# Kernel tuning notes

Measured on AMD Instinct MI355X. Metric: run time of the kernel, lower is better.

The kernel has to match this reference:

```python
import jax, jax.numpy as jnp
import numpy as np
from jax import lax

B, L, D_MODEL = 2, 4096, 1024
D_INNER = 2 * D_MODEL          # expand=2
D_STATE = D_INNER              # required: complex einsum contracts d_inner vs d_state
DT_RANK = 64                   # ceil(1024/16)
D_CONV = 4


def setup_inputs() -> dict:
    key = jax.random.key(0)
    ks = jax.random.split(key, 16)
    s = lambda *sh: 1.0 / np.sqrt(sh[-1])
    return {
        "hidden_states": jax.random.normal(ks[0], (B, L, D_MODEL), jnp.float32),
        "delta": jax.random.normal(ks[1], (B, L, DT_RANK), jnp.float32),
        # in_proj: Linear(d_model -> 2*d_inner), no bias
        "in_proj_w": jax.random.normal(ks[2], (2 * D_INNER, D_MODEL), jnp.float32) * s(D_MODEL),
        # depthwise causal conv1d: (out=d_inner, in/groups=1, k)
        "conv_w": jax.random.normal(ks[3], (D_INNER, 1, D_CONV), jnp.float32) * s(D_CONV),
        "conv_b": jax.random.normal(ks[4], (D_INNER,), jnp.float32) * 0.01,
        # ComplexStateSpace: only A_real affects the real output (x is real)
        "A_real": jax.random.normal(ks[5], (D_STATE, D_STATE), jnp.float32) * 0.1 / np.sqrt(D_STATE),
        # MIMO linears (torch Linear weight layout [out, in])
        "B_w": jax.random.normal(ks[6], (D_STATE, D_INNER), jnp.float32) * 0.1 * s(D_INNER),
        "C_w": jax.random.normal(ks[7], (D_INNER, D_STATE), jnp.float32) * 0.1 * s(D_STATE),
        "D_w": jax.random.normal(ks[8], (D_INNER, D_INNER), jnp.float32) * 0.1 * s(D_INNER),
        # SelectiveScan params
        "dt_proj_w": jax.random.normal(ks[9], (D_INNER, DT_RANK), jnp.float32) * 0.01,
        "dt_proj_b": jax.random.normal(ks[10], (D_INNER,), jnp.float32) * 0.01,
        "A_log": jax.random.uniform(ks[11], (D_INNER,), jnp.float32, -4.0, -1.0),
        "D_ss": jnp.ones((D_INNER,), jnp.float32),
        # out_proj: Linear(d_inner -> d_model), no bias
        "out_proj_w": jax.random.normal(ks[12], (D_MODEL, D_INNER), jnp.float32) * s(D_INNER),
    }


def reference(hidden_states, delta, in_proj_w, conv_w, conv_b, A_real,
              B_w, C_w, D_w, dt_proj_w, dt_proj_b, A_log, D_ss, out_proj_w):
    d_inner = A_log.shape[0]
    # in_proj + split
    xz = jnp.einsum('bld,ed->ble', hidden_states, in_proj_w)
    x, z = xz[..., :d_inner], xz[..., d_inner:]
    # depthwise causal conv1d (left-pad k-1 == torch pad both + truncate to L)
    xc = jnp.swapaxes(x, 1, 2)                      # [b, d, l]
    xc = lax.conv_general_dilated(xc, conv_w, window_strides=(1,),
                                  padding=[(D_CONV - 1, 0)],
                                  feature_group_count=d_inner)
    x = jnp.swapaxes(xc, 1, 2) + conv_b             # [b, l, d]
    x = jax.nn.silu(x)
    # ComplexStateSpace: real part of (x @ (A_real + iA_imag)) == x @ A_real
    x = x + jnp.einsum('bls,st->blt', x, A_real)
    # MIMO SSM: state_t = cumsum(B x)_t ; y_t = C state_t + D x_t  (vectorized)
    Bx = jnp.einsum('bld,sd->bls', x, B_w)          # [b, l, d_state]
    states = jnp.cumsum(Bx, axis=1)
    x_mimo = jnp.einsum('bls,es->ble', states, C_w) + jnp.einsum('bld,ed->ble', x, D_w)
    x = x + x_mimo
    # SelectiveScan: state = state * exp(dlt * A) + u, A = -exp(A_log)
    dlt = jax.nn.softplus(jnp.einsum('blr,dr->bld', delta, dt_proj_w) + dt_proj_b)
    decay = jnp.exp(dlt * (-jnp.exp(A_log)))        # [b, l, d], in (0, 1)

    def step(state, inp):
        dec, u = inp
        state = state * dec + u
        return state, state

    init = jnp.zeros_like(x[:, 0])
    _, scan_states = lax.scan(step, init,
                              (jnp.swapaxes(decay, 0, 1), jnp.swapaxes(x, 0, 1)))
    x = jnp.swapaxes(scan_states, 0, 1) + x * D_ss
    # gate + out projection
    out = x * jax.nn.silu(z)
    return jnp.einsum('ble,de->bld', out, out_proj_w)
```

## Files before the change

### kernel.cpp

```cpp
#include <hip/hip_runtime.h>
#include <cstdint>
#include <cstddef>


typedef unsigned short u16;
typedef __bf16 bf16x8 __attribute__((ext_vector_type(8)));
typedef float  f32x4  __attribute__((ext_vector_type(4)));

#define BDIM 256
#define M_ROWS 8192
#define LSEQ   4096
#define DI     2048
#define NCH    64
#define CLEN   64

__device__ __forceinline__ float bf2f(u16 h) {
    return __uint_as_float(((unsigned int)h) << 16);
}
__device__ __forceinline__ u16 f2bf(float f) {
    unsigned int u = __float_as_uint(f);
    u = u + 0x7fffu + ((u >> 16) & 1u);
    return (u16)(u >> 16);
}
__device__ __forceinline__ float siluf(float v) { return v / (1.0f + expf(-v)); }

__device__ __forceinline__ void load16_to_lds(const u16* g, u16* l) {
    __builtin_amdgcn_global_load_lds((const __attribute__((address_space(1))) void*)g,
                                     (__attribute__((address_space(3))) void*)l,
                                     16, 0, 0);
}

__global__ void k_cvt_all(const float* __restrict__ hs, const float* __restrict__ inproj,
                          const float* __restrict__ Bw, const float* __restrict__ Cw,
                          const float* __restrict__ outw, const float* __restrict__ delta,
                          const float* __restrict__ dtw,
                          u16* __restrict__ XH, u16* __restrict__ W1, u16* __restrict__ WBb,
                          u16* __restrict__ WC, u16* __restrict__ WO, u16* __restrict__ DLT,
                          u16* __restrict__ WDT) {
    long i = (long)(blockIdx.x * BDIM + threadIdx.x) * 4;
    const float* src; u16* dst; long off;
    if      (i <  8388608L) { src = hs;     dst = XH;  off = 0L; }
    else if (i < 12582912L) { src = inproj; dst = W1;  off = 8388608L; }
    else if (i < 16777216L) { src = Bw;     dst = WBb; off = 12582912L; }
    else if (i < 20971520L) { src = Cw;     dst = WC;  off = 16777216L; }
    else if (i < 23068672L) { src = outw;   dst = WO;  off = 20971520L; }
    else if (i < 23592960L) { src = delta;  dst = DLT; off = 23068672L; }
    else                    { src = dtw;    dst = WDT; off = 23592960L; }
    long j = i - off;
    float4 v = *reinterpret_cast<const float4*>(src + j);
    ushort2 a = {f2bf(v.x), f2bf(v.y)};
    ushort2 b = {f2bf(v.z), f2bf(v.w)};
    *reinterpret_cast<ushort2*>(dst + j)     = a;
    *reinterpret_cast<ushort2*>(dst + j + 2) = b;
}

__global__ void k_addI(const float* __restrict__ in, u16* __restrict__ out) {
    int i = (blockIdx.x * BDIM + threadIdx.x) * 4;
    int r = i >> 11, c = i & 2047;
    float4 v = *reinterpret_cast<const float4*>(in + i);
    if (r >= c && r < c + 4) (&v.x)[r - c] += 1.0f;
    ushort2 a = {f2bf(v.x), f2bf(v.y)};
    ushort2 b = {f2bf(v.z), f2bf(v.w)};
    *reinterpret_cast<ushort2*>(out + i)     = a;
    *reinterpret_cast<ushort2*>(out + i + 2) = b;
}

template <int MODE>
__global__ __launch_bounds__(256, 4)
void k_gemm(const u16* __restrict__ A1, const u16* __restrict__ W1, int K1,
            const u16* __restrict__ A2, const u16* __restrict__ W2, int K2,
            int N,
            float* __restrict__ outf, u16* __restrict__ outb,
            const float* __restrict__ bias1, const float* __restrict__ bias2) {
    __shared__ u16 As[128 * 64];
    __shared__ u16 Bs[128 * 64];
    const int tid  = threadIdx.x;
    const int wave = tid >> 6;
    const int lane = tid & 63;
    int bid  = blockIdx.x + gridDim.x * blockIdx.y;
    int nloc = (gridDim.x * gridDim.y) >> 3;
    int nid  = (bid & 7) * nloc + (bid >> 3);
    const int m0 = (nid / gridDim.x) * 128;
    const int n0 = (nid % gridDim.x) * 128;
    const int wm = (wave >> 1) * 64;
    const int wn = (wave & 1) * 64;
    const int lr = lane & 15;
    const int lq = lane >> 4;
    const int stg_row = lane >> 3;
    const int stg_col = (((lane & 7) ^ (lane >> 3)) << 3);

    f32x4 acc[4][4] = {};

    const int nt1 = K1 >> 6;
    const int nt2 = K2 >> 6;
    const int ntot = nt1 + nt2;

    for (int kt = 0; kt < ntot; ++kt) {
        const u16* Ap; const u16* Wp; int ld, k0;
        if (kt < nt1) { Ap = A1; Wp = W1; ld = K1; k0 = kt << 6; }
        else          { Ap = A2; Wp = W2; ld = K2; k0 = (kt - nt1) << 6; }
        #pragma unroll
        for (int i = 0; i < 4; ++i) {
            int chunk = wave * 4 + i;
            int r = chunk * 8 + stg_row;
            load16_to_lds(Ap + (size_t)(m0 + r) * ld + (k0 + stg_col), As + chunk * 512);
            load16_to_lds(Wp + (size_t)(n0 + r) * ld + (k0 + stg_col), Bs + chunk * 512);
        }
        __syncthreads();
        #pragma unroll
        for (int kk = 0; kk < 64; kk += 32) {
            bf16x8 af[4], bfr[4];
            #pragma unroll
            for (int i = 0; i < 4; ++i) {
                int R = wm + i * 16 + lr;
                af[i] = *reinterpret_cast<const bf16x8*>(
                    &As[R * 64 + ((kk + lq * 8) ^ ((R & 7) << 3))]);
            }
            #pragma unroll
            for (int i = 0; i < 4; ++i) {
                int R = wn + i * 16 + lr;
                bfr[i] = *reinterpret_cast<const bf16x8*>(
                    &Bs[R * 64 + ((kk + lq * 8) ^ ((R & 7) << 3))]);
            }
            #pragma unroll
            for (int mi = 0; mi < 4; ++mi)
                #pragma unroll
                for (int ni = 0; ni < 4; ++ni)
                    acc[mi][ni] = __builtin_amdgcn_mfma_f32_16x16x32_bf16(
                        af[mi], bfr[ni], acc[mi][ni], 0, 0, 0);
        }
        __syncthreads();
    }

    #pragma unroll
    for (int mi = 0; mi < 4; ++mi) {
        #pragma unroll
        for (int ni = 0; ni < 4; ++ni) {
            #pragma unroll
            for (int j = 0; j < 4; ++j) {
                int row = m0 + wm + mi * 16 + lq * 4 + j;
                int col = n0 + wn + ni * 16 + lr;
                size_t idx = (size_t)row * N + col;
                float v = acc[mi][ni][j];
                if constexpr (MODE == 5) {
                    float dlt = v + bias1[col];
                    dlt = (dlt > 15.f) ? dlt : log1pf(expf(dlt));
                    v = -expf(bias2[col]) * dlt;
                }
                if constexpr (MODE == 2) outf[idx] = v;
                else                     outb[idx] = f2bf(v);
            }
        }
    }
}

__global__ void k_conv(const u16* __restrict__ x, const float* __restrict__ w,
                       const float* __restrict__ b, u16* __restrict__ out) {
    int idx = blockIdx.x * BDIM + threadIdx.x;
    int d  = idx & (DI - 1);
    int bl = idx >> 11;
    int l  = bl & (LSEQ - 1);
    float4 wv = *reinterpret_cast<const float4*>(w + d * 4);
    float wj[4] = {wv.x, wv.y, wv.z, wv.w};
    float acc = b[d];
    #pragma unroll
    for (int j = 0; j < 4; ++j) {
        int ll = l - 3 + j;
        if (ll >= 0) acc += wj[j] * bf2f(x[(size_t)(bl - 3 + j) * DI + d]);
    }
    out[idx] = f2bf(siluf(acc));
}

__global__ void k_cumsum_p1(const u16* __restrict__ Bx, float* __restrict__ aux) {
    int t = blockIdx.x * BDIM + threadIdx.x;
    int s = t & (DI - 1);
    int c = (t >> 11) & (NCH - 1);
    int b = t >> 17;
    const u16* p = Bx + ((size_t)(b * LSEQ + c * CLEN) * DI) + s;
    float sum = 0.f;
    for (int i = 0; i < CLEN; ++i) sum += bf2f(p[(size_t)i * DI]);
    aux[t] = sum;
}
__global__ void k_cumsum_p2(const float* __restrict__ aux, float* __restrict__ carry) {
    int t = blockIdx.x * BDIM + threadIdx.x;
    int s = t & (DI - 1);
    int b = t >> 11;
    float run = 0.f;
    for (int c = 0; c < NCH; ++c) {
        int i = (b * NCH + c) * DI + s;
        carry[i] = run;
        run += aux[i];
    }
}
__global__ void k_cumsum_p3(const u16* __restrict__ Bx, const float* __restrict__ carry,
                            u16* __restrict__ st) {
    int t = blockIdx.x * BDIM + threadIdx.x;
    int s = t & (DI - 1);
    int c = (t >> 11) & (NCH - 1);
    int b = t >> 17;
    size_t base = ((size_t)(b * LSEQ + c * CLEN) * DI) + s;
    float run = carry[t];
    for (int i = 0; i < CLEN; ++i) {
        run += bf2f(Bx[base + (size_t)i * DI]);
        st[base + (size_t)i * DI] = f2bf(run);
    }
}

__global__ void k_scan_p1(const u16* __restrict__ ld_, const u16* __restrict__ u,
                          float* __restrict__ auxA, float* __restrict__ auxS) {
    int t = blockIdx.x * BDIM + threadIdx.x;
    int d = t & (DI - 1);
    int c = (t >> 11) & (NCH - 1);
    int b = t >> 17;
    size_t base = ((size_t)(b * LSEQ + c * CLEN) * DI) + d;
    float ap = 1.f, s = 0.f;
    for (int i = 0; i < CLEN; ++i) {
        size_t ix = base + (size_t)i * DI;
        float a = expf(bf2f(ld_[ix]));
        s = fmaf(a, s, bf2f(u[ix]));
        ap *= a;
    }
    auxA[t] = ap; auxS[t] = s;
}
__global__ void k_scan_p2(const float* __restrict__ auxA, const float* __restrict__ auxS,
                          float* __restrict__ carry) {
    int t = blockIdx.x * BDIM + threadIdx.x;
    int d = t & (DI - 1);
    int b = t >> 11;
    float run = 0.f;
    for (int c = 0; c < NCH; ++c) {
        int i = (b * NCH + c) * DI + d;
        carry[i] = run;
        run = fmaf(auxA[i], run, auxS[i]);
    }
}
__global__ void k_scan_p3(const u16* __restrict__ ld_, const u16* __restrict__ u,
                          const float* __restrict__ carry, const u16* __restrict__ z,
                          const float* __restrict__ Dss, u16* __restrict__ outb) {
    int t = blockIdx.x * BDIM + threadIdx.x;
    int d = t & (DI - 1);
    int c = (t >> 11) & (NCH - 1);
    int b = t >> 17;
    size_t base = ((size_t)(b * LSEQ + c * CLEN) * DI) + d;
    float s = carry[t];
    float dss = Dss[d];
    for (int i = 0; i < CLEN; ++i) {
        size_t ix = base + (size_t)i * DI;
        float a = expf(bf2f(ld_[ix]));
        float uu = bf2f(u[ix]);
        s = fmaf(a, s, uu);
        float x4 = s + uu * dss;
        float zz = bf2f(z[ix]);
        outb[ix] = f2bf(x4 * siluf(zz));
    }
}

extern "C" void kernel_launch(void* const* d_in, const int* in_sizes, int n_in,
                              void* d_out, int out_size, void* d_ws, size_t ws_size,
                              hipStream_t stream) {
    const float* hs     = (const float*)d_in[0];
    const float* delta  = (const float*)d_in[1];
    const float* inproj = (const float*)d_in[2];
    const float* convw  = (const float*)d_in[3];
    const float* convb  = (const float*)d_in[4];
    const float* Areal  = (const float*)d_in[5];
    const float* Bw     = (const float*)d_in[6];
    const float* Cw     = (const float*)d_in[7];
    const float* Dw     = (const float*)d_in[8];
    const float* dtw    = (const float*)d_in[9];
    const float* dtb    = (const float*)d_in[10];
    const float* Alog   = (const float*)d_in[11];
    const float* Dss    = (const float*)d_in[12];
    const float* outw   = (const float*)d_in[13];
    float* out = (float*)d_out;

    const size_t SZ_ACT = (size_t)M_ROWS * DI * 2;
    char* p = (char*)d_ws;
    u16* ZB  = (u16*)p; p += SZ_ACT;
    u16* XB  = (u16*)p;
    u16* X3  = XB;      p += SZ_ACT;
    u16* XC  = (u16*)p;
    u16* OUT = XC;      p += SZ_ACT;
    u16* BX  = (u16*)p;
    u16* LD  = BX;      p += SZ_ACT;
    u16* ST  = (u16*)p; p += SZ_ACT;
    u16* XH  = (u16*)p; p += (size_t)M_ROWS * 1024 * 2;
    u16* W1  = (u16*)p; p += (size_t)4096 * 1024 * 2;
    u16* WBb = (u16*)p; p += (size_t)DI * DI * 2;
    u16* WC  = (u16*)p; p += (size_t)DI * DI * 2;
    u16* Pb  = (u16*)p; p += (size_t)DI * DI * 2;
    u16* Db  = (u16*)p; p += (size_t)DI * DI * 2;
    u16* WBp = (u16*)p; p += (size_t)DI * DI * 2;
    u16* WXp = (u16*)p; p += (size_t)DI * DI * 2;
    u16* WO  = (u16*)p; p += (size_t)1024 * DI * 2;
    u16* WDT = (u16*)p; p += (size_t)DI * 64 * 2;
    u16* DLT = (u16*)p; p += (size_t)M_ROWS * 64 * 2;
    float* aux1 = (float*)p; p += (size_t)2 * NCH * DI * 4;
    float* aux2 = (float*)p; p += (size_t)2 * NCH * DI * 4;
    float* auxA = (float*)p; p += (size_t)2 * NCH * DI * 4;
    float* auxS = (float*)p; p += (size_t)2 * NCH * DI * 4;
    float* auxC = (float*)p; p += (size_t)2 * NCH * DI * 4;

    k_cvt_all<<<23168, BDIM, 0, stream>>>(hs, inproj, Bw, Cw, outw, delta, dtw,
                                          XH, W1, WBb, WC, WO, DLT, WDT);
    k_addI<<<4096, BDIM, 0, stream>>>(Areal, Pb);
    k_addI<<<4096, BDIM, 0, stream>>>(Dw, Db);

    k_gemm<0><<<dim3(16, 16), BDIM, 0, stream>>>(WBb, Pb, DI, nullptr, nullptr, 0,
                                                 DI, nullptr, WBp, nullptr, nullptr);
    k_gemm<0><<<dim3(16, 16), BDIM, 0, stream>>>(Db, Pb, DI, nullptr, nullptr, 0,
                                                 DI, nullptr, WXp, nullptr, nullptr);

    k_gemm<0><<<dim3(16, 64), BDIM, 0, stream>>>(XH, W1, 1024, nullptr, nullptr, 0,
                                                 DI, nullptr, XB, nullptr, nullptr);
    k_gemm<0><<<dim3(16, 64), BDIM, 0, stream>>>(XH, W1 + (size_t)DI * 1024, 1024,
                                                 nullptr, nullptr, 0,
                                                 DI, nullptr, ZB, nullptr, nullptr);
    k_conv<<<(M_ROWS * DI) / BDIM, BDIM, 0, stream>>>(XB, convw, convb, XC);
    k_gemm<0><<<dim3(16, 64), BDIM, 0, stream>>>(XC, WBp, DI, nullptr, nullptr, 0,
                                                 DI, nullptr, BX, nullptr, nullptr);
    k_cumsum_p1<<<(2 * NCH * DI) / BDIM, BDIM, 0, stream>>>(BX, aux1);
    k_cumsum_p2<<<(2 * DI) / BDIM, BDIM, 0, stream>>>(aux1, aux2);
    k_cumsum_p3<<<(2 * NCH * DI) / BDIM, BDIM, 0, stream>>>(BX, aux2, ST);
    k_gemm<5><<<dim3(16, 64), BDIM, 0, stream>>>(DLT, WDT, 64, nullptr, nullptr, 0,
                                                 DI, nullptr, LD, dtb, Alog);
    k_gemm<0><<<dim3(16, 64), BDIM, 0, stream>>>(ST, WC, DI, XC, WXp, DI,
                                                 DI, nullptr, X3, nullptr, nullptr);
    k_scan_p1<<<(2 * NCH * DI) / BDIM, BDIM, 0, stream>>>(LD, X3, auxA, auxS);
    k_scan_p2<<<(2 * DI) / BDIM, BDIM, 0, stream>>>(auxA, auxS, auxC);
    k_scan_p3<<<(2 * NCH * DI) / BDIM, BDIM, 0, stream>>>(LD, X3, auxC, ZB, Dss, OUT);
    k_gemm<2><<<dim3(8, 64), BDIM, 0, stream>>>(OUT, WO, DI, nullptr, nullptr, 0,
                                                1024, out, nullptr, nullptr, nullptr);
}
```

Baseline: 743.3 us.

## Batch independent GEMMs into grouped launches and fold scan carry passes

Merges the identity-add conversions into the single conversion kernel. Groups the independent GEMMs into two multi-tile launches: the two weight-premultiply GEMMs plus a combined in_proj with a split x/z epilogue, and the B-projection plus the dt projection. Removes the serial carry kernels of both chunked scans by having each chunk recompute its prefix from the per-chunk aggregates. The aim is to cut launch count and tail underutilisation, at the cost of redundant O(chunks) prefix work per thread and a runtime mode branch in the shared GEMM core.

```diff
diff --git a/kernel.cpp b/kernel.cpp
--- a/kernel.cpp
+++ b/kernel.cpp
@@ -33,55 +33,44 @@
 __global__ void k_cvt_all(const float* __restrict__ hs, const float* __restrict__ inproj,
                           const float* __restrict__ Bw, const float* __restrict__ Cw,
                           const float* __restrict__ outw, const float* __restrict__ delta,
-                          const float* __restrict__ dtw,
+                          const float* __restrict__ dtw, const float* __restrict__ Areal,
+                          const float* __restrict__ Dw,
                           u16* __restrict__ XH, u16* __restrict__ W1, u16* __restrict__ WBb,
                           u16* __restrict__ WC, u16* __restrict__ WO, u16* __restrict__ DLT,
-                          u16* __restrict__ WDT) {
+                          u16* __restrict__ WDT, u16* __restrict__ Pb, u16* __restrict__ Db) {
     long i = (long)(blockIdx.x * BDIM + threadIdx.x) * 4;
-    const float* src; u16* dst; long off;
+    const float* src; u16* dst; long off; bool diag = false;
     if      (i <  8388608L) { src = hs;     dst = XH;  off = 0L; }
     else if (i < 12582912L) { src = inproj; dst = W1;  off = 8388608L; }
     else if (i < 16777216L) { src = Bw;     dst = WBb; off = 12582912L; }
     else if (i < 20971520L) { src = Cw;     dst = WC;  off = 16777216L; }
     else if (i < 23068672L) { src = outw;   dst = WO;  off = 20971520L; }
     else if (i < 23592960L) { src = delta;  dst = DLT; off = 23068672L; }
-    else                    { src = dtw;    dst = WDT; off = 23592960L; }
+    else if (i < 23724032L) { src = dtw;    dst = WDT; off = 23592960L; }
+    else if (i < 27918336L) { src = Areal;  dst = Pb;  off = 23724032L; diag = true; }
+    else                    { src = Dw;     dst = Db;  off = 27918336L; diag = true; }
     long j = i - off;
     float4 v = *reinterpret_cast<const float4*>(src + j);
+    if (diag) {
+        int r = (int)(j >> 11), c = (int)(j & 2047);
+        if (r >= c && r < c + 4) (&v.x)[r - c] += 1.0f;
+    }
     ushort2 a = {f2bf(v.x), f2bf(v.y)};
     ushort2 b = {f2bf(v.z), f2bf(v.w)};
     *reinterpret_cast<ushort2*>(dst + j)     = a;
     *reinterpret_cast<ushort2*>(dst + j + 2) = b;
 }
 
-__global__ void k_addI(const float* __restrict__ in, u16* __restrict__ out) {
-    int i = (blockIdx.x * BDIM + threadIdx.x) * 4;
-    int r = i >> 11, c = i & 2047;
-    float4 v = *reinterpret_cast<const float4*>(in + i);
-    if (r >= c && r < c + 4) (&v.x)[r - c] += 1.0f;
-    ushort2 a = {f2bf(v.x), f2bf(v.y)};
-    ushort2 b = {f2bf(v.z), f2bf(v.w)};
-    *reinterpret_cast<ushort2*>(out + i)     = a;
-    *reinterpret_cast<ushort2*>(out + i + 2) = b;
-}
-
-template <int MODE>
-__global__ __launch_bounds__(256, 4)
-void k_gemm(const u16* __restrict__ A1, const u16* __restrict__ W1, int K1,
-            const u16* __restrict__ A2, const u16* __restrict__ W2, int K2,
-            int N,
-            float* __restrict__ outf, u16* __restrict__ outb,
-            const float* __restrict__ bias1, const float* __restrict__ bias2) {
-    __shared__ u16 As[128 * 64];
-    __shared__ u16 Bs[128 * 64];
+__device__ __forceinline__ void gemm_core(
+    u16* As, u16* Bs,
+    const u16* __restrict__ A1, const u16* __restrict__ W1, int K1,
+    const u16* __restrict__ A2, const u16* __restrict__ W2, int K2,
+    int N, float* __restrict__ outf, u16* __restrict__ outb, u16* __restrict__ outb2,
+    const float* __restrict__ bias1, const float* __restrict__ bias2,
+    int m0, int n0, int mode) {
     const int tid  = threadIdx.x;
     const int wave = tid >> 6;
     const int lane = tid & 63;
-    int bid  = blockIdx.x + gridDim.x * blockIdx.y;
-    int nloc = (gridDim.x * gridDim.y) >> 3;
-    int nid  = (bid & 7) * nloc + (bid >> 3);
-    const int m0 = (nid / gridDim.x) * 128;
-    const int n0 = (nid % gridDim.x) * 128;
     const int wm = (wave >> 1) * 64;
     const int wn = (wave & 1) * 64;
     const int lr = lane & 15;
@@ -140,18 +129,88 @@
             for (int j = 0; j < 4; ++j) {
                 int row = m0 + wm + mi * 16 + lq * 4 + j;
                 int col = n0 + wn + ni * 16 + lr;
-                size_t idx = (size_t)row * N + col;
                 float v = acc[mi][ni][j];
-                if constexpr (MODE == 5) {
+                if (mode == 6) {
+                    if (col < 2048) outb [(size_t)row * 2048 + col]        = f2bf(v);
+                    else            outb2[(size_t)row * 2048 + col - 2048] = f2bf(v);
+                } else if (mode == 5) {
                     float dlt = v + bias1[col];
                     dlt = (dlt > 15.f) ? dlt : log1pf(expf(dlt));
-                    v = -expf(bias2[col]) * dlt;
+                    outb[(size_t)row * N + col] = f2bf(-expf(bias2[col]) * dlt);
+                } else if (mode == 2) {
+                    outf[(size_t)row * N + col] = v;
+                } else {
+                    outb[(size_t)row * N + col] = f2bf(v);
                 }
-                if constexpr (MODE == 2) outf[idx] = v;
-                else                     outb[idx] = f2bf(v);
             }
         }
     }
+}
+
+__device__ __forceinline__ void tile_coords(int q, int T, int gn, int& m0, int& n0) {
+    int nloc = T >> 3;
+    int nid  = (q & 7) * nloc + (q >> 3);
+    m0 = (nid / gn) * 128;
+    n0 = (nid % gn) * 128;
+}
+
+__global__ __launch_bounds__(256, 4)
+void k_batch1(const u16* __restrict__ XH, const u16* __restrict__ W1,
+              const u16* __restrict__ WBb, const u16* __restrict__ Pb,
+              const u16* __restrict__ Db,
+              u16* __restrict__ WBp, u16* __restrict__ WXp,
+              u16* __restrict__ XB, u16* __restrict__ ZB) {
+    __shared__ u16 As[128 * 64];
+    __shared__ u16 Bs[128 * 64];
+    int bid = blockIdx.x;
+    int m0, n0;
+    if (bid < 256) {
+        tile_coords(bid, 256, 16, m0, n0);
+        gemm_core(As, Bs, WBb, Pb, DI, nullptr, nullptr, 0, DI,
+                  nullptr, WBp, nullptr, nullptr, nullptr, m0, n0, 0);
+    } else if (bid < 512) {
+        tile_coords(bid - 256, 256, 16, m0, n0);
+        gemm_core(As, Bs, Db, Pb, DI, nullptr, nullptr, 0, DI,
+                  nullptr, WXp, nullptr, nullptr, nullptr, m0, n0, 0);
+    } else {
+        tile_coords(bid - 512, 2048, 32, m0, n0);
+        gemm_core(As, Bs, XH, W1, 1024, nullptr, nullptr, 0, 4096,
+                  nullptr, XB, ZB, nullptr, nullptr, m0, n0, 6);
+    }
+}
+
+__global__ __launch_bounds__(256, 4)
+void k_batch2(const u16* __restrict__ XC, const u16* __restrict__ WBp,
+              const u16* __restrict__ DLT, const u16* __restrict__ WDT,
+              const float* __restrict__ dtb, const float* __restrict__ Alog,
+              u16* __restrict__ BX, u16* __restrict__ LD) {
+    __shared__ u16 As[128 * 64];
+    __shared__ u16 Bs[128 * 64];
+    int bid = blockIdx.x;
+    int m0, n0;
+    if (bid < 1024) {
+        tile_coords(bid, 1024, 16, m0, n0);
+        gemm_core(As, Bs, XC, WBp, DI, nullptr, nullptr, 0, DI,
+                  nullptr, BX, nullptr, nullptr, nullptr, m0, n0, 0);
+    } else {
+        tile_coords(bid - 1024, 1024, 16, m0, n0);
+        gemm_core(As, Bs, DLT, WDT, 64, nullptr, nullptr, 0, DI,
+                  nullptr, LD, nullptr, dtb, Alog, m0, n0, 5);
+    }
+}
+
+template <int MODE>
+__global__ __launch_bounds__(256, 4)
+void k_gemm(const u16* __restrict__ A1, const u16* __restrict__ W1, int K1,
+            const u16* __restrict__ A2, const u16* __restrict__ W2, int K2,
+            int N, float* __restrict__ outf, u16* __restrict__ outb) {
+    __shared__ u16 As[128 * 64];
+    __shared__ u16 Bs[128 * 64];
+    int bid = blockIdx.x + gridDim.x * blockIdx.y;
+    int m0, n0;
+    tile_coords(bid, gridDim.x * gridDim.y, gridDim.x, m0, n0);
+    gemm_core(As, Bs, A1, W1, K1, A2, W2, K2, N,
+              outf, outb, nullptr, nullptr, nullptr, m0, n0, MODE);
 }
 
 __global__ void k_conv(const u16* __restrict__ x, const float* __restrict__ w,
@@ -181,25 +240,15 @@
     for (int i = 0; i < CLEN; ++i) sum += bf2f(p[(size_t)i * DI]);
     aux[t] = sum;
 }
-__global__ void k_cumsum_p2(const float* __restrict__ aux, float* __restrict__ carry) {
-    int t = blockIdx.x * BDIM + threadIdx.x;
-    int s = t & (DI - 1);
-    int b = t >> 11;
-    float run = 0.f;
-    for (int c = 0; c < NCH; ++c) {
-        int i = (b * NCH + c) * DI + s;
-        carry[i] = run;
-        run += aux[i];
-    }
-}
-__global__ void k_cumsum_p3(const u16* __restrict__ Bx, const float* __restrict__ carry,
-                            u16* __restrict__ st) {
+__global__ void k_cumsum_p23(const u16* __restrict__ Bx, const float* __restrict__ aux,
+                             u16* __restrict__ st) {
     int t = blockIdx.x * BDIM + threadIdx.x;
     int s = t & (DI - 1);
     int c = (t >> 11) & (NCH - 1);
     int b = t >> 17;
+    float run = 0.f;
+    for (int j = 0; j < c; ++j) run += aux[(b * NCH + j) * DI + s];
     size_t base = ((size_t)(b * LSEQ + c * CLEN) * DI) + s;
-    float run = carry[t];
     for (int i = 0; i < CLEN; ++i) {
         run += bf2f(Bx[base + (size_t)i * DI]);
         st[base + (size_t)i * DI] = f2bf(run);
@@ -222,27 +271,20 @@
     }
     auxA[t] = ap; auxS[t] = s;
 }
-__global__ void k_scan_p2(const float* __restrict__ auxA, const float* __restrict__ auxS,
-                          float* __restrict__ carry) {
-    int t = blockIdx.x * BDIM + threadIdx.x;
-    int d = t & (DI - 1);
-    int b = t >> 11;
-    float run = 0.f;
-    for (int c = 0; c < NCH; ++c) {
-        int i = (b * NCH + c) * DI + d;
-        carry[i] = run;
-        run = fmaf(auxA[i], run, auxS[i]);
-    }
-}
-__global__ void k_scan_p3(const u16* __restrict__ ld_, const u16* __restrict__ u,
-                          const float* __restrict__ carry, const u16* __restrict__ z,
-                          const float* __restrict__ Dss, u16* __restrict__ outb) {
+__global__ void k_scan_p23(const u16* __restrict__ ld_, const u16* __restrict__ u,
+                           const float* __restrict__ auxA, const float* __restrict__ auxS,
+                           const u16* __restrict__ z, const float* __restrict__ Dss,
+                           u16* __restrict__ outb) {
     int t = blockIdx.x * BDIM + threadIdx.x;
     int d = t & (DI - 1);
     int c = (t >> 11) & (NCH - 1);
     int b = t >> 17;
+    float s = 0.f;
+    for (int j = 0; j < c; ++j) {
+        int i = (b * NCH + j) * DI + d;
+        s = fmaf(auxA[i], s, auxS[i]);
+    }
     size_t base = ((size_t)(b * LSEQ + c * CLEN) * DI) + d;
-    float s = carry[t];
     float dss = Dss[d];
     for (int i = 0; i < CLEN; ++i) {
         size_t ix = base + (size_t)i * DI;
@@ -281,10 +323,11 @@
     u16* X3  = XB;      p += SZ_ACT;
     u16* XC  = (u16*)p;
     u16* OUT = XC;      p += SZ_ACT;
-    u16* BX  = (u16*)p;
-    u16* LD  = BX;      p += SZ_ACT;
+    u16* BX  = (u16*)p; p += SZ_ACT;
     u16* ST  = (u16*)p; p += SZ_ACT;
-    u16* XH  = (u16*)p; p += (size_t)M_ROWS * 1024 * 2;
+    u16* XH  = (u16*)p;
+    u16* LD  = XH;
+                        p += (size_t)M_ROWS * 1024 * 2;
     u16* W1  = (u16*)p; p += (size_t)4096 * 1024 * 2;
     u16* WBb = (u16*)p; p += (size_t)DI * DI * 2;
     u16* WC  = (u16*)p; p += (size_t)DI * DI * 2;
@@ -296,39 +339,22 @@
     u16* WDT = (u16*)p; p += (size_t)DI * 64 * 2;
     u16* DLT = (u16*)p; p += (size_t)M_ROWS * 64 * 2;
     float* aux1 = (float*)p; p += (size_t)2 * NCH * DI * 4;
-    float* aux2 = (float*)p; p += (size_t)2 * NCH * DI * 4;
     float* auxA = (float*)p; p += (size_t)2 * NCH * DI * 4;
     float* auxS = (float*)p; p += (size_t)2 * NCH * DI * 4;
-    float* auxC = (float*)p; p += (size_t)2 * NCH * DI * 4;
-
-    k_cvt_all<<<23168, BDIM, 0, stream>>>(hs, inproj, Bw, Cw, outw, delta, dtw,
-                                          XH, W1, WBb, WC, WO, DLT, WDT);
-    k_addI<<<4096, BDIM, 0, stream>>>(Areal, Pb);
-    k_addI<<<4096, BDIM, 0, stream>>>(Dw, Db);
-
-    k_gemm<0><<<dim3(16, 16), BDIM, 0, stream>>>(WBb, Pb, DI, nullptr, nullptr, 0,
-                                                 DI, nullptr, WBp, nullptr, nullptr);
-    k_gemm<0><<<dim3(16, 16), BDIM, 0, stream>>>(Db, Pb, DI, nullptr, nullptr, 0,
-                                                 DI, nullptr, WXp, nullptr, nullptr);
-
-    k_gemm<0><<<dim3(16, 64), BDIM, 0, stream>>>(XH, W1, 1024, nullptr, nullptr, 0,
-                                                 DI, nullptr, XB, nullptr, nullptr);
-    k_gemm<0><<<dim3(16, 64), BDIM, 0, stream>>>(XH, W1 + (size_t)DI * 1024, 1024,
-                                                 nullptr, nullptr, 0,
-                                                 DI, nullptr, ZB, nullptr, nullptr);
+
+    k_cvt_all<<<31360, BDIM, 0, stream>>>(hs, inproj, Bw, Cw, outw, delta, dtw,
+                                          Areal, Dw,
+                                          XH, W1, WBb, WC, WO, DLT, WDT, Pb, Db);
+    k_batch1<<<2560, BDIM, 0, stream>>>(XH, W1, WBb, Pb, Db, WBp, WXp, XB, ZB);
     k_conv<<<(M_ROWS * DI) / BDIM, BDIM, 0, stream>>>(XB, convw, convb, XC);
-    k_gemm<0><<<dim3(16, 64), BDIM, 0, stream>>>(XC, WBp, DI, nullptr, nullptr, 0,
-                                                 DI, nullptr, BX, nullptr, nullptr);
+    k_batch2<<<2048, BDIM, 0, stream>>>(XC, WBp, DLT, WDT, dtb, Alog, BX, LD);
     k_cumsum_p1<<<(2 * NCH * DI) / BDIM, BDIM, 0, stream>>>(BX, aux1);
-    k_cumsum_p2<<<(2 * DI) / BDIM, BDIM, 0, stream>>>(aux1, aux2);
-    k_cumsum_p3<<<(2 * NCH * DI) / BDIM, BDIM, 0, stream>>>(BX, aux2, ST);
-    k_gemm<5><<<dim3(16, 64), BDIM, 0, stream>>>(DLT, WDT, 64, nullptr, nullptr, 0,
-                                                 DI, nullptr, LD, dtb, Alog);
+    k_cumsum_p23<<<(2 * NCH * DI) / BDIM, BDIM, 0, stream>>>(BX, aux1, ST);
     k_gemm<0><<<dim3(16, 64), BDIM, 0, stream>>>(ST, WC, DI, XC, WXp, DI,
-                                                 DI, nullptr, X3, nullptr, nullptr);
+                                                 DI, nullptr, X3);
     k_scan_p1<<<(2 * NCH * DI) / BDIM, BDIM, 0, stream>>>(LD, X3, auxA, auxS);
-    k_scan_p2<<<(2 * DI) / BDIM, BDIM, 0, stream>>>(auxA, auxS, auxC);
-    k_scan_p3<<<(2 * NCH * DI) / BDIM, BDIM, 0, stream>>>(LD, X3, auxC, ZB, Dss, OUT);
+    k_scan_p23<<<(2 * NCH * DI) / BDIM, BDIM, 0, stream>>>(LD, X3, auxA, auxS,
+                                                           ZB, Dss, OUT);
     k_gemm<2><<<dim3(8, 64), BDIM, 0, stream>>>(OUT, WO, DI, nullptr, nullptr, 0,
-                                                1024, out, nullptr, nullptr, nullptr);
-}
+                                                1024, out, nullptr);
+}
```

New measurement: 703.9 us. -5.3%, faster.
